# Kernel optimization log

Measured on AMD Instinct MI355X. Metric: run time of the kernel, lower is better.

The kernel has to match this reference:

```python
import jax, jax.numpy as jnp
import numpy as np

FIELDS = 32
EMBED = 64
PAIRS = FIELDS * (FIELDS - 1) // 2  # 496
BATCH = 2048


def setup_inputs() -> dict:
    key = jax.random.key(0)
    k1, k2 = jax.random.split(key)
    x = jax.random.normal(k1, (BATCH, FIELDS, EMBED), dtype=jnp.float32)
    kernel = jax.random.normal(k2, (EMBED, PAIRS, EMBED), dtype=jnp.float32) * 0.05
    return {"x": x, "kernel": kernel}


def reference(x, kernel):
    # Pair enumeration (i<j) matching the python double loop order.
    iu, ju = jnp.triu_indices(FIELDS, k=1)
    p = x[:, iu, :]  # (B, P, E)
    q = x[:, ju, :]  # (B, P, E)
    # Original: kp[b,f,pr] = sum_e p[b,pr,e]*kernel[f,pr,e];
    # result[b,pr] = sum_f kp[b,f,pr]*q[b,pr,f]
    # => bilinear form per pair, fused as a single einsum.
    result = jnp.einsum('bpe,fpe,bpf->bp', p, kernel, q)
    return result
```

## Files before the change

kernel.cpp:

```cpp
#include <hip/hip_runtime.h>
#include <hip/hip_bf16.h>


constexpr int BATCH  = 2048;
constexpr int FIELDS = 32;
constexpr int EMBED  = 64;
constexpr int PAIRS  = FIELDS * (FIELDS - 1) / 2;

typedef __attribute__((ext_vector_type(8))) short  short8;
typedef __attribute__((ext_vector_type(4))) float  f32x4;

constexpr size_t XN      = (size_t)BATCH * FIELDS * EMBED;
constexpr size_t KPN     = (size_t)PAIRS * 2 * 4 * 64 * 8;
constexpr size_t XH_OFF  = 0;
constexpr size_t XL_OFF  = XH_OFF + XN * 2;
constexpr size_t KPH_OFF = XL_OFF + XN * 2;
constexpr size_t KPL_OFF = KPH_OFF + KPN * 2;
constexpr size_t WS_NEED = KPL_OFF + KPN * 2;

__device__ __forceinline__ unsigned short f32_to_bf16_rne(float f) {
    unsigned int u = __float_as_uint(f);
    u = u + 0x7fffu + ((u >> 16) & 1u);
    return (unsigned short)(u >> 16);
}
__device__ __forceinline__ float bf16_bits_to_f32(unsigned short h) {
    return __uint_as_float(((unsigned int)h) << 16);
}

__global__ __launch_bounds__(256) void convert_x_kernel(
    const float* __restrict__ x,
    unsigned short* __restrict__ xh,
    unsigned short* __restrict__ xl)
{
    const int idx = (int)blockIdx.x * 256 + (int)threadIdx.x;
    const float4 v = ((const float4*)x)[idx];
    const float vv[4] = {v.x, v.y, v.z, v.w};
    unsigned short h[4], l[4];
    #pragma unroll
    for (int j = 0; j < 4; ++j) {
        const unsigned short hb = f32_to_bf16_rne(vv[j]);
        h[j] = hb;
        l[j] = f32_to_bf16_rne(vv[j] - bf16_bits_to_f32(hb));
    }
    ((ushort4*)xh)[idx] = make_ushort4(h[0], h[1], h[2], h[3]);
    ((ushort4*)xl)[idx] = make_ushort4(l[0], l[1], l[2], l[3]);
}

__global__ __launch_bounds__(256) void pack_k_kernel(
    const float* __restrict__ kern,
    unsigned short* __restrict__ kph,
    unsigned short* __restrict__ kpl)
{
    const int t    = (int)blockIdx.x * 256 + (int)threadIdx.x;
    const int lane = t & 63;
    const int nc   = (t >> 6) & 3;
    const int ks   = (t >> 8) & 1;
    const int pair = t >> 9;
    const int e    = nc * 16 + (lane & 15);
    const int f0   = ks * 32 + (lane >> 4) * 8;

    unsigned short h[8], l[8];
    #pragma unroll
    for (int jj = 0; jj < 8; ++jj) {
        const float v = kern[((size_t)(f0 + jj) * PAIRS + pair) * EMBED + e];
        const unsigned short hb = f32_to_bf16_rne(v);
        h[jj] = hb;
        l[jj] = f32_to_bf16_rne(v - bf16_bits_to_f32(hb));
    }
    #pragma unroll
    for (int jj = 0; jj < 8; ++jj) {
        kph[(size_t)t * 8 + jj] = h[jj];
        kpl[(size_t)t * 8 + jj] = l[jj];
    }
}

__global__ __launch_bounds__(256) void opn_mfma_kernel(
    const float* __restrict__ x,
    const unsigned short* __restrict__ xh,
    const unsigned short* __restrict__ xl,
    const unsigned short* __restrict__ kph,
    const unsigned short* __restrict__ kpl,
    float* __restrict__ out)
{
    const int bid  = (int)blockIdx.x;
    const int p    = bid >> 3;
    const int mt   = bid & 7;
    const int wave = (int)threadIdx.x >> 6;
    const int lane = (int)threadIdx.x & 63;
    const int Mb   = mt * 256 + wave * 64;
    const int g    = lane >> 4;
    const int c    = lane & 15;

    int i = 0, rem = p;
    while (rem >= FIELDS - 1 - i) { rem -= FIELDS - 1 - i; ++i; }
    const int jf = i + 1 + rem;

    f32x4 acc[4][4];
    #pragma unroll
    for (int mr = 0; mr < 4; ++mr)
        #pragma unroll
        for (int nc = 0; nc < 4; ++nc)
            acc[mr][nc] = (f32x4){0.f, 0.f, 0.f, 0.f};

    #pragma unroll
    for (int ks = 0; ks < 2; ++ks) {
        short8 ah[4], al[4];
        #pragma unroll
        for (int mr = 0; mr < 4; ++mr) {
            const int row = Mb + mr * 16 + c;
            const size_t off = ((size_t)row * FIELDS + jf) * EMBED + ks * 32 + g * 8;
            ah[mr] = *(const short8*)(xh + off);
            al[mr] = *(const short8*)(xl + off);
        }
        short8 bh[4], bl[4];
        #pragma unroll
        for (int nc = 0; nc < 4; ++nc) {
            const size_t kidx = (((size_t)(p * 2 + ks) * 4 + nc) * 64 + lane) * 8;
            bh[nc] = *(const short8*)(kph + kidx);
            bl[nc] = *(const short8*)(kpl + kidx);
        }
        #pragma unroll
        for (int mr = 0; mr < 4; ++mr) {
            #pragma unroll
            for (int nc = 0; nc < 4; ++nc) {
                acc[mr][nc] = __builtin_amdgcn_mfma_f32_16x16x32_bf16(ah[mr], bh[nc], acc[mr][nc], 0, 0, 0);
                acc[mr][nc] = __builtin_amdgcn_mfma_f32_16x16x32_bf16(ah[mr], bl[nc], acc[mr][nc], 0, 0, 0);
                acc[mr][nc] = __builtin_amdgcn_mfma_f32_16x16x32_bf16(al[mr], bh[nc], acc[mr][nc], 0, 0, 0);
            }
        }
    }

    float z[4][4];
    #pragma unroll
    for (int mr = 0; mr < 4; ++mr)
        #pragma unroll
        for (int t = 0; t < 4; ++t)
            z[mr][t] = 0.f;

    const size_t xi_base = (size_t)i * EMBED + c;
    #pragma unroll
    for (int mr = 0; mr < 4; ++mr) {
        #pragma unroll
        for (int t = 0; t < 4; ++t) {
            const int row = Mb + mr * 16 + 4 * g + t;
            const float* xi = x + (size_t)row * (FIELDS * EMBED) + xi_base;
            #pragma unroll
            for (int nc = 0; nc < 4; ++nc)
                z[mr][t] = fmaf(acc[mr][nc][t], xi[nc * 16], z[mr][t]);
        }
    }

    #pragma unroll
    for (int mask = 1; mask < 16; mask <<= 1) {
        #pragma unroll
        for (int mr = 0; mr < 4; ++mr)
            #pragma unroll
            for (int t = 0; t < 4; ++t)
                z[mr][t] += __shfl_xor(z[mr][t], mask, 64);
    }

    if (c < 4) {
        const int t = c;
        #pragma unroll
        for (int mr = 0; mr < 4; ++mr) {
            const int row = Mb + mr * 16 + 4 * g + t;
            out[(size_t)row * PAIRS + p] = z[mr][t];
        }
    }
}

constexpr int BT     = 64;
constexpr int BTILES = BATCH / BT;

__global__ __launch_bounds__(64) void opn_fp32_kernel(
    const float* __restrict__ x,
    const float* __restrict__ kern,
    float* __restrict__ out)
{
    const int bid   = (int)blockIdx.x;
    const int p     = bid >> 5;
    const int btile = bid & (BTILES - 1);
    const int lane  = (int)threadIdx.x;
    const int b     = btile * BT + lane;

    int i = 0, rem = p;
    while (rem >= FIELDS - 1 - i) { rem -= FIELDS - 1 - i; ++i; }
    const int j = i + 1 + rem;

    const float* xrow_i = x + (size_t)b * (FIELDS * EMBED) + i * EMBED;
    const float* xrow_j = x + (size_t)b * (FIELDS * EMBED) + j * EMBED;
    const float* kp     = kern + (size_t)p * EMBED;

    float acc[EMBED];
    #pragma unroll
    for (int e = 0; e < EMBED; ++e) acc[e] = 0.0f;

    const float4* xj4 = (const float4*)xrow_j;
    #pragma unroll 2
    for (int f4 = 0; f4 < EMBED / 4; ++f4) {
        const float4 v = xj4[f4];
        const float xjf[4] = {v.x, v.y, v.z, v.w};
        #pragma unroll
        for (int s = 0; s < 4; ++s) {
            const float* kf = kp + (size_t)(f4 * 4 + s) * (PAIRS * EMBED);
            #pragma unroll
            for (int e = 0; e < EMBED; ++e)
                acc[e] = fmaf(xjf[s], kf[e], acc[e]);
        }
    }

    float r = 0.0f;
    const float4* xi4 = (const float4*)xrow_i;
    #pragma unroll
    for (int e4 = 0; e4 < EMBED / 4; ++e4) {
        const float4 u = xi4[e4];
        r = fmaf(u.x, acc[e4 * 4 + 0], r);
        r = fmaf(u.y, acc[e4 * 4 + 1], r);
        r = fmaf(u.z, acc[e4 * 4 + 2], r);
        r = fmaf(u.w, acc[e4 * 4 + 3], r);
    }
    out[(size_t)b * PAIRS + p] = r;
}

extern "C" void kernel_launch(void* const* d_in, const int* in_sizes, int n_in,
                              void* d_out, int out_size, void* d_ws, size_t ws_size,
                              hipStream_t stream) {
    const float* x    = (const float*)d_in[0];
    const float* kern = (const float*)d_in[1];
    float*       out  = (float*)d_out;

    if (ws_size < WS_NEED) {
        opn_fp32_kernel<<<dim3(PAIRS * BTILES), dim3(64), 0, stream>>>(x, kern, out);
        return;
    }

    char* ws = (char*)d_ws;
    unsigned short* xhi = (unsigned short*)(ws + XH_OFF);
    unsigned short* xlo = (unsigned short*)(ws + XL_OFF);
    unsigned short* kph = (unsigned short*)(ws + KPH_OFF);
    unsigned short* kpl = (unsigned short*)(ws + KPL_OFF);

    convert_x_kernel<<<dim3((unsigned)(XN / 4 / 256)), dim3(256), 0, stream>>>(x, xhi, xlo);
    pack_k_kernel<<<dim3((unsigned)(PAIRS * 2 * 4 * 64 / 256)), dim3(256), 0, stream>>>(kern, kph, kpl);
    opn_mfma_kernel<<<dim3(PAIRS * 8), dim3(256), 0, stream>>>(x, xhi, xlo, kph, kpl, out);
}
```

Measured before the change: 126.5 us.

## Fuse x bf16 hi/lo split into MFMA kernel, drop separate conversion pass

Removes the separate convert_x kernel and its 32 MB of workspace traffic. The MFMA kernel now loads fp32 x rows directly and splits them into bf16 hi/lo in registers. All B fragments for both k-steps are loaded up front, and the kernel gets launch_bounds(256,1). pack_k now writes vectorized short8 stores. Register pressure rises, and the fp32 loads of x are twice as wide per element, in exchange for one fewer launch and no intermediate buffer.

```diff
diff --git a/kernel.cpp b/kernel.cpp
--- a/kernel.cpp
+++ b/kernel.cpp
@@ -10,12 +10,9 @@
 typedef __attribute__((ext_vector_type(8))) short  short8;
 typedef __attribute__((ext_vector_type(4))) float  f32x4;
 
-constexpr size_t XN      = (size_t)BATCH * FIELDS * EMBED;
 constexpr size_t KPN     = (size_t)PAIRS * 2 * 4 * 64 * 8;
-constexpr size_t XH_OFF  = 0;
-constexpr size_t XL_OFF  = XH_OFF + XN * 2;
-constexpr size_t KPH_OFF = XL_OFF + XN * 2;
-constexpr size_t KPL_OFF = KPH_OFF + KPN * 2;
+constexpr size_t KPH_OFF = 0;
+constexpr size_t KPL_OFF = KPN * 2;
 constexpr size_t WS_NEED = KPL_OFF + KPN * 2;
 
 __device__ __forceinline__ unsigned short f32_to_bf16_rne(float f) {
@@ -26,24 +23,13 @@
 __device__ __forceinline__ float bf16_bits_to_f32(unsigned short h) {
     return __uint_as_float(((unsigned int)h) << 16);
 }
-
-__global__ __launch_bounds__(256) void convert_x_kernel(
-    const float* __restrict__ x,
-    unsigned short* __restrict__ xh,
-    unsigned short* __restrict__ xl)
-{
-    const int idx = (int)blockIdx.x * 256 + (int)threadIdx.x;
-    const float4 v = ((const float4*)x)[idx];
-    const float vv[4] = {v.x, v.y, v.z, v.w};
-    unsigned short h[4], l[4];
-    #pragma unroll
-    for (int j = 0; j < 4; ++j) {
-        const unsigned short hb = f32_to_bf16_rne(vv[j]);
-        h[j] = hb;
-        l[j] = f32_to_bf16_rne(vv[j] - bf16_bits_to_f32(hb));
-    }
-    ((ushort4*)xh)[idx] = make_ushort4(h[0], h[1], h[2], h[3]);
-    ((ushort4*)xl)[idx] = make_ushort4(l[0], l[1], l[2], l[3]);
+__device__ __forceinline__ void split8(const float* v, short8& h8, short8& l8) {
+    #pragma unroll
+    for (int j = 0; j < 8; ++j) {
+        const unsigned short hb = f32_to_bf16_rne(v[j]);
+        h8[j] = (short)hb;
+        l8[j] = (short)f32_to_bf16_rne(v[j] - bf16_bits_to_f32(hb));
+    }
 }
 
 __global__ __launch_bounds__(256) void pack_k_kernel(
@@ -59,25 +45,19 @@
     const int e    = nc * 16 + (lane & 15);
     const int f0   = ks * 32 + (lane >> 4) * 8;
 
-    unsigned short h[8], l[8];
-    #pragma unroll
-    for (int jj = 0; jj < 8; ++jj) {
-        const float v = kern[((size_t)(f0 + jj) * PAIRS + pair) * EMBED + e];
-        const unsigned short hb = f32_to_bf16_rne(v);
-        h[jj] = hb;
-        l[jj] = f32_to_bf16_rne(v - bf16_bits_to_f32(hb));
-    }
-    #pragma unroll
-    for (int jj = 0; jj < 8; ++jj) {
-        kph[(size_t)t * 8 + jj] = h[jj];
-        kpl[(size_t)t * 8 + jj] = l[jj];
-    }
-}
-
-__global__ __launch_bounds__(256) void opn_mfma_kernel(
+    float v[8];
+    #pragma unroll
+    for (int jj = 0; jj < 8; ++jj)
+        v[jj] = kern[((size_t)(f0 + jj) * PAIRS + pair) * EMBED + e];
+
+    short8 h8, l8;
+    split8(v, h8, l8);
+    *(short8*)(kph + (size_t)t * 8) = h8;
+    *(short8*)(kpl + (size_t)t * 8) = l8;
+}
+
+__global__ __launch_bounds__(256, 1) void opn_mfma_kernel(
     const float* __restrict__ x,
-    const unsigned short* __restrict__ xh,
-    const unsigned short* __restrict__ xl,
     const unsigned short* __restrict__ kph,
     const unsigned short* __restrict__ kpl,
     float* __restrict__ out)
@@ -95,6 +75,37 @@
     while (rem >= FIELDS - 1 - i) { rem -= FIELDS - 1 - i; ++i; }
     const int jf = i + 1 + rem;
 
+    float4 xa[4][2][2];
+    #pragma unroll
+    for (int mr = 0; mr < 4; ++mr) {
+        const int row = Mb + mr * 16 + c;
+        const float* base = x + ((size_t)row * FIELDS + jf) * EMBED;
+        #pragma unroll
+        for (int ks = 0; ks < 2; ++ks) {
+            xa[mr][ks][0] = *(const float4*)(base + ks * 32 + g * 8);
+            xa[mr][ks][1] = *(const float4*)(base + ks * 32 + g * 8 + 4);
+        }
+    }
+    short8 bh[2][4], bl[2][4];
+    #pragma unroll
+    for (int ks = 0; ks < 2; ++ks)
+        #pragma unroll
+        for (int nc = 0; nc < 4; ++nc) {
+            const size_t kidx = (((size_t)(p * 2 + ks) * 4 + nc) * 64 + lane) * 8;
+            bh[ks][nc] = *(const short8*)(kph + kidx);
+            bl[ks][nc] = *(const short8*)(kpl + kidx);
+        }
+
+    short8 ah[4][2], al[4][2];
+    #pragma unroll
+    for (int mr = 0; mr < 4; ++mr)
+        #pragma unroll
+        for (int ks = 0; ks < 2; ++ks) {
+            const float4 a0 = xa[mr][ks][0], a1 = xa[mr][ks][1];
+            const float v[8] = {a0.x, a0.y, a0.z, a0.w, a1.x, a1.y, a1.z, a1.w};
+            split8(v, ah[mr][ks], al[mr][ks]);
+        }
+
     f32x4 acc[4][4];
     #pragma unroll
     for (int mr = 0; mr < 4; ++mr)
@@ -103,32 +114,15 @@
             acc[mr][nc] = (f32x4){0.f, 0.f, 0.f, 0.f};
 
     #pragma unroll
-    for (int ks = 0; ks < 2; ++ks) {
-        short8 ah[4], al[4];
-        #pragma unroll
-        for (int mr = 0; mr < 4; ++mr) {
-            const int row = Mb + mr * 16 + c;
-            const size_t off = ((size_t)row * FIELDS + jf) * EMBED + ks * 32 + g * 8;
-            ah[mr] = *(const short8*)(xh + off);
-            al[mr] = *(const short8*)(xl + off);
-        }
-        short8 bh[4], bl[4];
-        #pragma unroll
-        for (int nc = 0; nc < 4; ++nc) {
-            const size_t kidx = (((size_t)(p * 2 + ks) * 4 + nc) * 64 + lane) * 8;
-            bh[nc] = *(const short8*)(kph + kidx);
-            bl[nc] = *(const short8*)(kpl + kidx);
-        }
-        #pragma unroll
-        for (int mr = 0; mr < 4; ++mr) {
+    for (int ks = 0; ks < 2; ++ks)
+        #pragma unroll
+        for (int mr = 0; mr < 4; ++mr)
             #pragma unroll
             for (int nc = 0; nc < 4; ++nc) {
-                acc[mr][nc] = __builtin_amdgcn_mfma_f32_16x16x32_bf16(ah[mr], bh[nc], acc[mr][nc], 0, 0, 0);
-                acc[mr][nc] = __builtin_amdgcn_mfma_f32_16x16x32_bf16(ah[mr], bl[nc], acc[mr][nc], 0, 0, 0);
-                acc[mr][nc] = __builtin_amdgcn_mfma_f32_16x16x32_bf16(al[mr], bh[nc], acc[mr][nc], 0, 0, 0);
+                acc[mr][nc] = __builtin_amdgcn_mfma_f32_16x16x32_bf16(ah[mr][ks], bh[ks][nc], acc[mr][nc], 0, 0, 0);
+                acc[mr][nc] = __builtin_amdgcn_mfma_f32_16x16x32_bf16(ah[mr][ks], bl[ks][nc], acc[mr][nc], 0, 0, 0);
+                acc[mr][nc] = __builtin_amdgcn_mfma_f32_16x16x32_bf16(al[mr][ks], bh[ks][nc], acc[mr][nc], 0, 0, 0);
             }
-        }
-    }
 
     float z[4][4];
     #pragma unroll
@@ -139,7 +133,7 @@
 
     const size_t xi_base = (size_t)i * EMBED + c;
     #pragma unroll
-    for (int mr = 0; mr < 4; ++mr) {
+    for (int mr = 0; mr < 4; ++mr)
         #pragma unroll
         for (int t = 0; t < 4; ++t) {
             const int row = Mb + mr * 16 + 4 * g + t;
@@ -148,16 +142,14 @@
             for (int nc = 0; nc < 4; ++nc)
                 z[mr][t] = fmaf(acc[mr][nc][t], xi[nc * 16], z[mr][t]);
         }
-    }
-
-    #pragma unroll
-    for (int mask = 1; mask < 16; mask <<= 1) {
+
+    #pragma unroll
+    for (int mask = 1; mask < 16; mask <<= 1)
         #pragma unroll
         for (int mr = 0; mr < 4; ++mr)
             #pragma unroll
             for (int t = 0; t < 4; ++t)
                 z[mr][t] += __shfl_xor(z[mr][t], mask, 64);
-    }
 
     if (c < 4) {
         const int t = c;
@@ -235,12 +227,9 @@
     }
 
     char* ws = (char*)d_ws;
-    unsigned short* xhi = (unsigned short*)(ws + XH_OFF);
-    unsigned short* xlo = (unsigned short*)(ws + XL_OFF);
     unsigned short* kph = (unsigned short*)(ws + KPH_OFF);
     unsigned short* kpl = (unsigned short*)(ws + KPL_OFF);
 
-    convert_x_kernel<<<dim3((unsigned)(XN / 4 / 256)), dim3(256), 0, stream>>>(x, xhi, xlo);
-    pack_k_kernel<<<dim3((unsigned)(PAIRS * 2 * 4 * 64 / 256)), dim3(256), 0, stream>>>(kern, kph, kpl);
-    opn_mfma_kernel<<<dim3(PAIRS * 8), dim3(256), 0, stream>>>(x, xhi, xlo, kph, kpl, out);
-}
+    pack_k_kernel<<<dim3(PAIRS * 512 / 256), dim3(256), 0, stream>>>(kern, kph, kpl);
+    opn_mfma_kernel<<<dim3(PAIRS * 8), dim3(256), 0, stream>>>(x, kph, kpl, out);
+}
```

Result: no change. 125.3 us (-1.0%).
